# Kernel tuning notes

Measured on AMD Instinct MI355X. Metric: run time of the kernel, lower is better.

The kernel has to match this reference:

```python
import jax, jax.numpy as jnp
import numpy as np

B, N, C = 4, 4096, 1024
E = 8
K = 2
HIGH = 2            # high_noise_experts
THRESH = 0.5        # snr_threshold
CAP_FACTOR = 1.25
INTER = C * 8 // 3  # 2730


def setup_inputs() -> dict:
    key = jax.random.key(0)
    k = jax.random.split(key, 6)
    return {
        "x": jax.random.normal(k[0], (B, N, C), jnp.float32),
        "cond": jax.random.normal(k[1], (B, C), jnp.float32),
        "snr": jax.random.uniform(k[2], (B,), jnp.float32),
        "gate_w": jax.random.normal(k[3], (2 * C, E), jnp.float32) * 0.02,
        "gate_up_w": jax.random.normal(k[4], (E, C, 2 * INTER), jnp.float32) * 0.02,
        "down_w": jax.random.normal(k[5], (E, INTER, C), jnp.float32) * 0.02,
    }


def _moe_forward(x, cond, snr, gate_w, gate_up_w, down_w):
    b, n, c = x.shape
    x_flat = x.reshape(b * n, c)                       # (T, C)
    cond_flat = jnp.repeat(cond, n, axis=0)            # (T, C)
    snr_flat = jnp.repeat(snr, n)                      # (T,)

    # gating: concat(content, conditioning) -> expert logits
    logits = jnp.concatenate([x_flat, cond_flat], axis=-1) @ gate_w  # (T, E)

    # SNR mask: high-noise tokens may only use experts [0, HIGH)
    high_noise = (snr_flat < THRESH)[:, None]          # (T, 1)
    low_noise_cols = jnp.arange(E) >= HIGH             # (E,)
    logits = logits + jnp.where(high_noise & low_noise_cols, -jnp.inf, 0.0)

    # eval mode: no jitter noise
    probs = jax.nn.softmax(logits, axis=-1)            # (T, E)
    top_probs, top_idx = jax.lax.top_k(probs, K)       # (T, K)
    top_probs = top_probs / jnp.maximum(top_probs.sum(-1, keepdims=True), 1e-12)

    T = b * n
    capacity = max(1, int(CAP_FACTOR * T / E))

    def expert_fn(e, wgu, wd):
        # priority of each (token, slot) for expert e; unassigned -> -inf
        pri = jnp.where(top_idx == e, top_probs, -jnp.inf).reshape(-1)  # (T*K,)
        vals, idx = jax.lax.top_k(pri, capacity)       # capacity-limited select
        tok = idx // K                                 # token index of each slot
        w = jnp.where(jnp.isfinite(vals), vals, 0.0)   # zero weight for padding
        xe = x_flat[tok]                               # (cap, C) gather
        gu = xe @ wgu                                  # (cap, 2*INTER)
        g, u = jnp.split(gu, 2, axis=-1)
        y = (jax.nn.silu(g) * u) @ wd                  # (cap, C)
        return tok, y * w[:, None]

    toks, ys = jax.vmap(expert_fn)(jnp.arange(E), gate_up_w, down_w)
    out = jnp.zeros_like(x_flat).at[toks.reshape(-1)].add(ys.reshape(-1, c))
    return out.reshape(b, n, c)


def reference(x, cond, snr, gate_w, gate_up_w, down_w):
    out = _moe_forward(x, cond, snr, gate_w, gate_up_w, down_w)
    # eval mode: load-balance loss is 0
    return out, jnp.float32(0.0)
```

## Files before the change

### kernel.cpp

```cpp
#include <hip/hip_runtime.h>
#include <hip/hip_bf16.h>
#include <stdint.h>

#define T_TOK 16384
#define CDIM  1024
#define ENUM_ 8
#define INTER_ 2730
#define IPAD  2752
#define NGU   5460
#define NGUPAD 5504
#define CAP   2560
#define EGRP  4
#define CSTRIDE 64

typedef __attribute__((ext_vector_type(8))) short short8;
typedef __attribute__((ext_vector_type(4))) float f32x4;
typedef unsigned long long u64;
typedef unsigned int u32;

static __device__ __forceinline__ ushort f2bf(float f){
  u32 u = __float_as_uint(f);
  u32 r = u + 0x7FFFu + ((u >> 16) & 1u);
  return (ushort)(r >> 16);
}

static __device__ __forceinline__ void glds16(const void* g, void* l){
  __builtin_amdgcn_global_load_lds(
      (const __attribute__((address_space(1))) void*)g,
      (__attribute__((address_space(3))) void*)l, 16, 0, 0);
}

__global__ void k_tr_wgu(const float* __restrict__ wgu, ushort* __restrict__ wguT){
  __shared__ float tile[32][33];
  const int e = blockIdx.z;
  const int k0 = blockIdx.x*32, n0 = blockIdx.y*32;
  const float* src = wgu + (size_t)e*CDIM*NGU;
  ushort* dst = wguT + (size_t)e*NGUPAD*CDIM;
  const int tx = threadIdx.x, ty = threadIdx.y;
  #pragma unroll
  for (int r = ty; r < 32; r += 8){
    int n = n0 + tx;
    int j = (n < IPAD) ? n : n - (IPAD - INTER_);
    bool valid = (n < INTER_) || (n >= IPAD && j < NGU);
    tile[r][tx] = valid ? src[(size_t)(k0 + r)*NGU + j] : 0.f;
  }
  __syncthreads();
  #pragma unroll
  for (int r = ty; r < 32; r += 8)
    dst[(size_t)(n0 + r)*CDIM + k0 + tx] = f2bf(tile[tx][r]);
}

__global__ void k_tr_dwn(const float* __restrict__ dw, ushort* __restrict__ dwT){
  __shared__ float tile[32][33];
  const int e = blockIdx.z;
  const int k0 = blockIdx.x*32, n0 = blockIdx.y*32;
  const float* src = dw + (size_t)e*INTER_*CDIM;
  ushort* dst = dwT + (size_t)e*CDIM*IPAD;
  const int tx = threadIdx.x, ty = threadIdx.y;
  #pragma unroll
  for (int r = ty; r < 32; r += 8){
    int k = k0 + r;
    tile[r][tx] = (k < INTER_) ? src[(size_t)k*CDIM + n0 + tx] : 0.f;
  }
  __syncthreads();
  #pragma unroll
  for (int r = ty; r < 32; r += 8)
    dst[(size_t)(n0 + r)*IPAD + k0 + tx] = f2bf(tile[tx][r]);
}

__global__ void k_cond(const float* __restrict__ cond, const float* __restrict__ gate_w,
                       float* __restrict__ condlog){
  const int b = blockIdx.x;
  const int wave = threadIdx.x >> 6, lane = threadIdx.x & 63;
  float a0 = 0.f, a1 = 0.f;
  for (int c = lane; c < CDIM; c += 64){
    float cv = cond[(size_t)b*CDIM + c];
    const float* g = gate_w + (size_t)(CDIM + c)*8;
    a0 += cv * g[2*wave]; a1 += cv * g[2*wave + 1];
  }
  #pragma unroll
  for (int off = 32; off; off >>= 1){
    a0 += __shfl_down(a0, off, 64);
    a1 += __shfl_down(a1, off, 64);
  }
  if (lane == 0){
    condlog[b*8 + 2*wave]     = a0;
    condlog[b*8 + 2*wave + 1] = a1;
  }
}

__global__ __launch_bounds__(256) void k_gate(
    const float* __restrict__ x, const float* __restrict__ gate_w,
    const float* __restrict__ condlog, const float* __restrict__ snr,
    u32* __restrict__ pcnt, u64* __restrict__ entries, ushort* __restrict__ xb){
  __shared__ float gwT[8*1024];
  __shared__ u32 lcnt[8];
  __shared__ u32 lbase[8];
  __shared__ u64 keybuf[32];
  __shared__ u32 posbuf[32];
  const int tid = threadIdx.x;
  if (tid < 8) lcnt[tid] = 0;
  for (int idx = tid; idx < 8192; idx += 256){
    float v = gate_w[idx];
    gwT[(idx & 7)*1024 + (idx >> 3)] = v;
  }
  __syncthreads();
  const int wave = tid >> 6, lane = tid & 63;
  const int tbase = blockIdx.x*16 + wave*4;
  #pragma unroll 1
  for (int it = 0; it < 4; ++it){
    const int t = tbase + it;
    const int b = t >> 12;
    float acc[8] = {0,0,0,0,0,0,0,0};
    #pragma unroll
    for (int i = 0; i < 4; ++i){
      const int c = lane*4 + 256*i;
      const float4 xv = *(const float4*)(x + (size_t)t*CDIM + c);
      ushort4 xo;
      xo.x = f2bf(xv.x); xo.y = f2bf(xv.y); xo.z = f2bf(xv.z); xo.w = f2bf(xv.w);
      *(ushort4*)(xb + (size_t)t*CDIM + c) = xo;
      #pragma unroll
      for (int e = 0; e < 8; ++e){
        const float4 gv = *(const float4*)(gwT + e*1024 + c);
        acc[e] += xv.x*gv.x + xv.y*gv.y + xv.z*gv.z + xv.w*gv.w;
      }
    }
    #pragma unroll
    for (int e = 0; e < 8; ++e)
      #pragma unroll
      for (int off = 32; off; off >>= 1)
        acc[e] += __shfl_down(acc[e], off, 64);
    if (lane == 0){
      bool hn = snr[b] < 0.5f;
      float lg[8];
      #pragma unroll
      for (int e = 0; e < 8; ++e) lg[e] = acc[e] + condlog[b*8 + e];
      float mx = -1e30f;
      #pragma unroll
      for (int e = 0; e < 8; ++e) if (!(hn && e >= 2) && lg[e] > mx) mx = lg[e];
      float p[8]; float s = 0.f;
      #pragma unroll
      for (int e = 0; e < 8; ++e){ p[e] = (hn && e >= 2) ? 0.f : expf(lg[e] - mx); s += p[e]; }
      float inv = 1.f / s;
      #pragma unroll
      for (int e = 0; e < 8; ++e) p[e] *= inv;
      int i0 = 0;
      #pragma unroll
      for (int e = 1; e < 8; ++e) if (p[e] > p[i0]) i0 = e;
      int i1 = -1; float pv1 = -1.f;
      #pragma unroll
      for (int e = 0; e < 8; ++e) if (e != i0 && p[e] > pv1){ pv1 = p[e]; i1 = e; }
      float v0 = p[i0], v1 = pv1;
      float den = fmaxf(v0 + v1, 1e-12f);
      v0 /= den; v1 /= den;
      u32 flat0 = (u32)(t*2);
      const int slot = wave*4 + it;
      u32 p0 = atomicAdd(&lcnt[i0], 1u);
      u32 p1 = atomicAdd(&lcnt[i1], 1u);
      keybuf[2*slot]     = ((u64)__float_as_uint(v0) << 32) | (u64)(0xFFFFFFFFu - flat0);
      posbuf[2*slot]     = ((u32)i0 << 16) | p0;
      keybuf[2*slot + 1] = ((u64)__float_as_uint(v1) << 32) | (u64)(0xFFFFFFFFu - (flat0 + 1u));
      posbuf[2*slot + 1] = ((u32)i1 << 16) | p1;
    }
  }
  __syncthreads();
  if (tid < 8) lbase[tid] = atomicAdd(&pcnt[tid*CSTRIDE], lcnt[tid]);
  __syncthreads();
  if (tid < 32){
    u32 pe = posbuf[tid];
    int e = (int)(pe >> 16);
    u32 pos = pe & 0xFFFFu;
    entries[(size_t)e*T_TOK + lbase[e] + pos] = keybuf[tid];
  }
}

__global__ void k_select(const u32* __restrict__ pcnt, const u64* __restrict__ entries,
                         u64* __restrict__ thresh){
  const int e = blockIdx.x;
  const int n = (int)pcnt[e*CSTRIDE];
  if (n <= CAP){ if (threadIdx.x == 0) thresh[e] = 0ull; return; }
  const u64* keys = entries + (size_t)e*T_TOK;
  __shared__ u32 hist[256];
  __shared__ u64 spfx;
  __shared__ int srem;
  u64 prefix = 0, pmask = 0;
  int rem = CAP;
  for (int d = 7; d >= 0; --d){
    const int sh = d*8;
    hist[threadIdx.x] = 0;
    __syncthreads();
    for (int i = threadIdx.x; i < n; i += 256){
      u64 k = keys[i];
      if ((k & pmask) == prefix)
        atomicAdd(&hist[(u32)((k >> sh) & 0xFFull)], 1u);
    }
    __syncthreads();
    if (threadIdx.x == 0){
      int c = 0, chosen = 0, nr = rem;
      for (int v = 255; v >= 0; --v){
        int nc = c + (int)hist[v];
        if (nc >= rem){ chosen = v; nr = rem - c; break; }
        c = nc;
      }
      spfx = prefix | ((u64)(u32)chosen << sh);
      srem = nr;
    }
    __syncthreads();
    prefix = spfx; rem = srem; pmask |= (0xFFull << sh);
  }
  if (threadIdx.x == 0) thresh[e] = prefix;
}

__global__ void k_compact(const u32* __restrict__ pcnt, const u64* __restrict__ entries,
                          const u64* __restrict__ thresh, u32* __restrict__ mcnt,
                          int* __restrict__ tokbuf, float* __restrict__ wgtbuf){
  const int e = blockIdx.y;
  const int n = (int)pcnt[e*CSTRIDE];
  const u64 th = thresh[e];
  const u64* keys = entries + (size_t)e*T_TOK;
  for (int i = blockIdx.x*256 + threadIdx.x; i < n; i += gridDim.x*256){
    u64 k = keys[i];
    if (k >= th){
      u32 pos = atomicAdd(&mcnt[e], 1u);
      u32 flat = 0xFFFFFFFFu - (u32)(k & 0xFFFFFFFFull);
      tokbuf[(size_t)e*CAP + pos] = (int)(flat >> 1);
      wgtbuf[(size_t)e*CAP + pos] = __uint_as_float((u32)(k >> 32));
    }
  }
}

__global__ __launch_bounds__(256) void k_gemm1(
    const ushort* __restrict__ xb, const ushort* __restrict__ wguT_g,
    const int* __restrict__ tok_g, const u32* __restrict__ mcnt_g,
    ushort* __restrict__ h_g){
  const int z = blockIdx.z;
  const int m_e = (int)mcnt_g[z];
  const int m0 = blockIdx.x * 128;
  if (m0 >= m_e) return;
  const ushort* wguT = wguT_g + (size_t)z*NGUPAD*CDIM;
  const int* tok = tok_g + (size_t)z*CAP;
  ushort* h = h_g + (size_t)z*CAP*IPAD;
  const int j0 = blockIdx.y * 64;

  __shared__ ushort As[128*32];
  __shared__ ushort Bg[64*32];
  __shared__ ushort Bu[64*32];
  const int tid = threadIdx.x;
  const int lane = tid & 63, wave = tid >> 6;
  const int wm = wave >> 1, wn = wave & 1;
  const int lm = lane & 15, quad = lane >> 4;

  const int af0 = tid*8, af1 = tid*8 + 2048;
  const ushort* ag0 = xb + (size_t)tok[m0 + (af0 >> 5)]*CDIM + (af0 & 31);
  const ushort* ag1 = xb + (size_t)tok[m0 + (af1 >> 5)]*CDIM + (af1 & 31);
  const int br = tid >> 2, bc = (tid & 3)*8;
  const ushort* bgp = wguT + (size_t)(j0 + br)*CDIM + bc;
  const ushort* bup = wguT + (size_t)(IPAD + j0 + br)*CDIM + bc;

  f32x4 accg[4][2], accu[4][2];
  #pragma unroll
  for (int i = 0; i < 4; ++i)
    #pragma unroll
    for (int j = 0; j < 2; ++j){
      accg[i][j] = (f32x4){0.f,0.f,0.f,0.f};
      accu[i][j] = (f32x4){0.f,0.f,0.f,0.f};
    }

  for (int k0 = 0; k0 < CDIM; k0 += 32){
    glds16(ag0 + k0, As + af0);
    glds16(ag1 + k0, As + af1);
    glds16(bgp + k0, Bg + tid*8);
    glds16(bup + k0, Bu + tid*8);
    __syncthreads();
    short8 a[4], vg[2], vu[2];
    #pragma unroll
    for (int mt = 0; mt < 4; ++mt)
      a[mt] = *(const short8*)(As + (wm*64 + mt*16 + lm)*32 + quad*8);
    #pragma unroll
    for (int nt = 0; nt < 2; ++nt){
      vg[nt] = *(const short8*)(Bg + (wn*32 + nt*16 + lm)*32 + quad*8);
      vu[nt] = *(const short8*)(Bu + (wn*32 + nt*16 + lm)*32 + quad*8);
    }
    __syncthreads();
    #pragma unroll
    for (int mt = 0; mt < 4; ++mt)
      #pragma unroll
      for (int nt = 0; nt < 2; ++nt){
        accg[mt][nt] = __builtin_amdgcn_mfma_f32_16x16x32_bf16(a[mt], vg[nt], accg[mt][nt], 0, 0, 0);
        accu[mt][nt] = __builtin_amdgcn_mfma_f32_16x16x32_bf16(a[mt], vu[nt], accu[mt][nt], 0, 0, 0);
      }
  }
  #pragma unroll
  for (int mt = 0; mt < 4; ++mt)
    #pragma unroll
    for (int nt = 0; nt < 2; ++nt)
      #pragma unroll
      for (int r = 0; r < 4; ++r){
        int row = m0 + wm*64 + mt*16 + quad*4 + r;
        int col = j0 + wn*32 + nt*16 + lm;
        float g = accg[mt][nt][r];
        float uu = accu[mt][nt][r];
        float sg = g / (1.f + __expf(-g));
        h[(size_t)row*IPAD + col] = f2bf(sg * uu);
      }
}

__global__ __launch_bounds__(256) void k_gemm2(
    const ushort* __restrict__ h_g, const ushort* __restrict__ dwT_g,
    const int* __restrict__ tok_g, const float* __restrict__ wgt_g,
    const u32* __restrict__ mcnt_g, float* __restrict__ out){
  const int z = blockIdx.z;
  const int m_e = (int)mcnt_g[z];
  const int m0 = blockIdx.x * 128;
  if (m0 >= m_e) return;
  const ushort* h = h_g + (size_t)z*CAP*IPAD;
  const ushort* dwT = dwT_g + (size_t)z*CDIM*IPAD;
  const int* tok = tok_g + (size_t)z*CAP;
  const float* wgt = wgt_g + (size_t)z*CAP;
  const int n0 = blockIdx.y * 128;

  __shared__ ushort As[128*32];
  __shared__ ushort Bs[128*32];
  const int tid = threadIdx.x;
  const int lane = tid & 63, wave = tid >> 6;
  const int wm = wave >> 1, wn = wave & 1;
  const int lm = lane & 15, quad = lane >> 4;

  const int af0 = tid*8, af1 = tid*8 + 2048;
  const ushort* ap0 = h + (size_t)(m0 + (af0 >> 5))*IPAD + (af0 & 31);
  const ushort* ap1 = h + (size_t)(m0 + (af1 >> 5))*IPAD + (af1 & 31);
  const ushort* bp0 = dwT + (size_t)(n0 + (af0 >> 5))*IPAD + (af0 & 31);
  const ushort* bp1 = dwT + (size_t)(n0 + (af1 >> 5))*IPAD + (af1 & 31);

  f32x4 acc[4][4];
  #pragma unroll
  for (int i = 0; i < 4; ++i)
    #pragma unroll
    for (int j = 0; j < 4; ++j) acc[i][j] = (f32x4){0.f,0.f,0.f,0.f};

  for (int k0 = 0; k0 < IPAD; k0 += 32){
    glds16(ap0 + k0, As + af0);
    glds16(ap1 + k0, As + af1);
    glds16(bp0 + k0, Bs + af0);
    glds16(bp1 + k0, Bs + af1);
    __syncthreads();
    short8 a[4], b[4];
    #pragma unroll
    for (int mt = 0; mt < 4; ++mt)
      a[mt] = *(const short8*)(As + (wm*64 + mt*16 + lm)*32 + quad*8);
    #pragma unroll
    for (int nt = 0; nt < 4; ++nt)
      b[nt] = *(const short8*)(Bs + (wn*64 + nt*16 + lm)*32 + quad*8);
    __syncthreads();
    #pragma unroll
    for (int mt = 0; mt < 4; ++mt)
      #pragma unroll
      for (int nt = 0; nt < 4; ++nt)
        acc[mt][nt] = __builtin_amdgcn_mfma_f32_16x16x32_bf16(a[mt], b[nt], acc[mt][nt], 0, 0, 0);
  }
  #pragma unroll
  for (int mt = 0; mt < 4; ++mt)
    #pragma unroll
    for (int r = 0; r < 4; ++r){
      int row = m0 + wm*64 + mt*16 + quad*4 + r;
      float w = wgt[row];
      float* orow = out + (size_t)tok[row]*CDIM;
      #pragma unroll
      for (int nt = 0; nt < 4; ++nt){
        int col = n0 + wn*64 + nt*16 + lm;
        atomicAdd(orow + col, w * acc[mt][nt][r]);
      }
    }
}

extern "C" void kernel_launch(void* const* d_in, const int* in_sizes, int n_in,
                              void* d_out, int out_size, void* d_ws, size_t ws_size,
                              hipStream_t stream){
  const float* x      = (const float*)d_in[0];
  const float* cond   = (const float*)d_in[1];
  const float* snr    = (const float*)d_in[2];
  const float* gate_w = (const float*)d_in[3];
  const float* wgu    = (const float*)d_in[4];
  const float* wdn    = (const float*)d_in[5];
  float* out = (float*)d_out;
  (void)in_sizes; (void)n_in; (void)ws_size;

  char* ws = (char*)d_ws;
  size_t off = 0;
  auto take = [&](size_t bytes) -> char* {
    char* p = ws + off;
    off += (bytes + 255) & ~(size_t)255;
    return p;
  };
  u32* pcnt     = (u32*)take(8*CSTRIDE*4);
  u32* mcnt     = (u32*)take(256);
  float* condlog = (float*)take(256);
  u64* thresh   = (u64*)take(256);
  u64* entries  = (u64*)take((size_t)ENUM_*T_TOK*8);
  int* tokbuf   = (int*)take((size_t)ENUM_*CAP*4);
  float* wgtbuf = (float*)take((size_t)ENUM_*CAP*4);
  ushort* xb    = (ushort*)take((size_t)T_TOK*CDIM*2);
  ushort* wguT  = (ushort*)take((size_t)ENUM_*NGUPAD*CDIM*2);
  ushort* dwT   = (ushort*)take((size_t)ENUM_*CDIM*IPAD*2);
  ushort* hbuf  = (ushort*)take((size_t)EGRP*CAP*IPAD*2);

  hipMemsetAsync(pcnt, 0, 8*CSTRIDE*4, stream);
  hipMemsetAsync(mcnt, 0, 256, stream);
  hipMemsetAsync(tokbuf, 0, (size_t)ENUM_*CAP*4, stream);
  hipMemsetAsync(wgtbuf, 0, (size_t)ENUM_*CAP*4, stream);
  hipMemsetAsync(out, 0, (size_t)out_size*sizeof(float), stream);

  k_cond<<<4, 256, 0, stream>>>(cond, gate_w, condlog);
  k_gate<<<T_TOK/16, 256, 0, stream>>>(x, gate_w, condlog, snr, pcnt, entries, xb);
  k_tr_wgu<<<dim3(CDIM/32, NGUPAD/32, ENUM_), dim3(32,8), 0, stream>>>(wgu, wguT);
  k_tr_dwn<<<dim3(IPAD/32, CDIM/32, ENUM_), dim3(32,8), 0, stream>>>(wdn, dwT);
  k_select<<<ENUM_, 256, 0, stream>>>(pcnt, entries, thresh);
  k_compact<<<dim3(64, ENUM_), 256, 0, stream>>>(pcnt, entries, thresh, mcnt, tokbuf, wgtbuf);

  for (int g = 0; g < ENUM_/EGRP; ++g){
    k_gemm1<<<dim3(CAP/128, IPAD/64, EGRP), 256, 0, stream>>>(
        xb, wguT + (size_t)g*EGRP*NGUPAD*CDIM,
        tokbuf + (size_t)g*EGRP*CAP, mcnt + g*EGRP, hbuf);
    k_gemm2<<<dim3(CAP/128, CDIM/128, EGRP), 256, 0, stream>>>(
        hbuf, dwT + (size_t)g*EGRP*CDIM*IPAD,
        tokbuf + (size_t)g*EGRP*CAP, wgtbuf + (size_t)g*EGRP*CAP,
        mcnt + g*EGRP, out);
  }
}
```

Baseline: 1.045 ms.

## Replace atomic scatter-add in down-proj with per-expert buffer and token gather

The down-projection GEMM now writes unweighted per-expert outputs to a dense fp32 buffer instead of atomically adding weighted rows into the output. The compact kernel records an inverse map from each token to its (expert, slot) entries, and a new gather kernel sums the weighted rows per token and writes each output row once. This removes the float atomics and the output memset, and it merges several memsets into one range. The cost is an extra 80MB fp32 intermediate written and read back, plus one more kernel launch.

```diff
diff --git a/kernel.cpp b/kernel.cpp
--- a/kernel.cpp
+++ b/kernel.cpp
@@ -141,9 +141,9 @@
       float p[8]; float s = 0.f;
       #pragma unroll
       for (int e = 0; e < 8; ++e){ p[e] = (hn && e >= 2) ? 0.f : expf(lg[e] - mx); s += p[e]; }
-      float inv = 1.f / s;
-      #pragma unroll
-      for (int e = 0; e < 8; ++e) p[e] *= inv;
+      float inv_ = 1.f / s;
+      #pragma unroll
+      for (int e = 0; e < 8; ++e) p[e] *= inv_;
       int i0 = 0;
       #pragma unroll
       for (int e = 1; e < 8; ++e) if (p[e] > p[i0]) i0 = e;
@@ -213,7 +213,8 @@
 
 __global__ void k_compact(const u32* __restrict__ pcnt, const u64* __restrict__ entries,
                           const u64* __restrict__ thresh, u32* __restrict__ mcnt,
-                          int* __restrict__ tokbuf, float* __restrict__ wgtbuf){
+                          int* __restrict__ tokbuf, float* __restrict__ wgtbuf,
+                          u32* __restrict__ invcnt, u32* __restrict__ inv){
   const int e = blockIdx.y;
   const int n = (int)pcnt[e*CSTRIDE];
   const u64 th = thresh[e];
@@ -223,8 +224,11 @@
     if (k >= th){
       u32 pos = atomicAdd(&mcnt[e], 1u);
       u32 flat = 0xFFFFFFFFu - (u32)(k & 0xFFFFFFFFull);
-      tokbuf[(size_t)e*CAP + pos] = (int)(flat >> 1);
+      int t = (int)(flat >> 1);
+      tokbuf[(size_t)e*CAP + pos] = t;
       wgtbuf[(size_t)e*CAP + pos] = __uint_as_float((u32)(k >> 32));
+      u32 ic = atomicAdd(&invcnt[t], 1u);
+      inv[2*t + ic] = ((u32)e << 12) | pos;
     }
   }
 }
@@ -307,16 +311,13 @@
 
 __global__ __launch_bounds__(256) void k_gemm2(
     const ushort* __restrict__ h_g, const ushort* __restrict__ dwT_g,
-    const int* __restrict__ tok_g, const float* __restrict__ wgt_g,
-    const u32* __restrict__ mcnt_g, float* __restrict__ out){
+    const u32* __restrict__ mcnt_g, float* __restrict__ y_g){
   const int z = blockIdx.z;
   const int m_e = (int)mcnt_g[z];
   const int m0 = blockIdx.x * 128;
   if (m0 >= m_e) return;
   const ushort* h = h_g + (size_t)z*CAP*IPAD;
   const ushort* dwT = dwT_g + (size_t)z*CDIM*IPAD;
-  const int* tok = tok_g + (size_t)z*CAP;
-  const float* wgt = wgt_g + (size_t)z*CAP;
   const int n0 = blockIdx.y * 128;
 
   __shared__ ushort As[128*32];
@@ -363,14 +364,41 @@
     #pragma unroll
     for (int r = 0; r < 4; ++r){
       int row = m0 + wm*64 + mt*16 + quad*4 + r;
-      float w = wgt[row];
-      float* orow = out + (size_t)tok[row]*CDIM;
+      float* yrow = y_g + ((size_t)z*CAP + row)*CDIM;
       #pragma unroll
       for (int nt = 0; nt < 4; ++nt){
         int col = n0 + wn*64 + nt*16 + lm;
-        atomicAdd(orow + col, w * acc[mt][nt][r]);
+        yrow[col] = acc[mt][nt][r];
       }
     }
+}
+
+__global__ __launch_bounds__(256) void k_out(
+    const float* __restrict__ ybuf, const u32* __restrict__ inv,
+    const u32* __restrict__ invcnt, const float* __restrict__ wgtbuf,
+    float* __restrict__ out){
+  const int t = blockIdx.x*4 + (threadIdx.x >> 6);
+  const int lane = threadIdx.x & 63;
+  const int n = (int)invcnt[t];
+  f32x4 acc[4];
+  #pragma unroll
+  for (int i = 0; i < 4; ++i) acc[i] = (f32x4){0.f,0.f,0.f,0.f};
+  for (int j = 0; j < n; ++j){
+    u32 v = inv[2*t + j];
+    int e = (int)(v >> 12);
+    int pos = (int)(v & 0xFFFu);
+    float w = wgtbuf[e*CAP + pos];
+    const float* yr = ybuf + ((size_t)e*CAP + pos)*CDIM;
+    #pragma unroll
+    for (int i = 0; i < 4; ++i){
+      f32x4 yv = *(const f32x4*)(yr + i*256 + lane*4);
+      acc[i] += yv * w;
+    }
+  }
+  float* orow = out + (size_t)t*CDIM;
+  #pragma unroll
+  for (int i = 0; i < 4; ++i)
+    *(f32x4*)(orow + i*256 + lane*4) = acc[i];
 }
 
 extern "C" void kernel_launch(void* const* d_in, const int* in_sizes, int n_in,
@@ -383,7 +411,7 @@
   const float* wgu    = (const float*)d_in[4];
   const float* wdn    = (const float*)d_in[5];
   float* out = (float*)d_out;
-  (void)in_sizes; (void)n_in; (void)ws_size;
+  (void)in_sizes; (void)n_in; (void)ws_size; (void)out_size;
 
   char* ws = (char*)d_ws;
   size_t off = 0;
@@ -396,6 +424,8 @@
   u32* mcnt     = (u32*)take(256);
   float* condlog = (float*)take(256);
   u64* thresh   = (u64*)take(256);
+  u32* invcnt   = (u32*)take((size_t)T_TOK*4);
+  u32* inv      = (u32*)take((size_t)T_TOK*2*4);
   u64* entries  = (u64*)take((size_t)ENUM_*T_TOK*8);
   int* tokbuf   = (int*)take((size_t)ENUM_*CAP*4);
   float* wgtbuf = (float*)take((size_t)ENUM_*CAP*4);
@@ -403,19 +433,18 @@
   ushort* wguT  = (ushort*)take((size_t)ENUM_*NGUPAD*CDIM*2);
   ushort* dwT   = (ushort*)take((size_t)ENUM_*CDIM*IPAD*2);
   ushort* hbuf  = (ushort*)take((size_t)EGRP*CAP*IPAD*2);
-
-  hipMemsetAsync(pcnt, 0, 8*CSTRIDE*4, stream);
-  hipMemsetAsync(mcnt, 0, 256, stream);
+  float* ybuf   = (float*)take((size_t)ENUM_*CAP*CDIM*4);
+
+  hipMemsetAsync(pcnt, 0, 68352, stream);
   hipMemsetAsync(tokbuf, 0, (size_t)ENUM_*CAP*4, stream);
-  hipMemsetAsync(wgtbuf, 0, (size_t)ENUM_*CAP*4, stream);
-  hipMemsetAsync(out, 0, (size_t)out_size*sizeof(float), stream);
 
   k_cond<<<4, 256, 0, stream>>>(cond, gate_w, condlog);
   k_gate<<<T_TOK/16, 256, 0, stream>>>(x, gate_w, condlog, snr, pcnt, entries, xb);
   k_tr_wgu<<<dim3(CDIM/32, NGUPAD/32, ENUM_), dim3(32,8), 0, stream>>>(wgu, wguT);
   k_tr_dwn<<<dim3(IPAD/32, CDIM/32, ENUM_), dim3(32,8), 0, stream>>>(wdn, dwT);
   k_select<<<ENUM_, 256, 0, stream>>>(pcnt, entries, thresh);
-  k_compact<<<dim3(64, ENUM_), 256, 0, stream>>>(pcnt, entries, thresh, mcnt, tokbuf, wgtbuf);
+  k_compact<<<dim3(64, ENUM_), 256, 0, stream>>>(pcnt, entries, thresh, mcnt,
+                                                 tokbuf, wgtbuf, invcnt, inv);
 
   for (int g = 0; g < ENUM_/EGRP; ++g){
     k_gemm1<<<dim3(CAP/128, IPAD/64, EGRP), 256, 0, stream>>>(
@@ -423,7 +452,7 @@
         tokbuf + (size_t)g*EGRP*CAP, mcnt + g*EGRP, hbuf);
     k_gemm2<<<dim3(CAP/128, CDIM/128, EGRP), 256, 0, stream>>>(
         hbuf, dwT + (size_t)g*EGRP*CDIM*IPAD,
-        tokbuf + (size_t)g*EGRP*CAP, wgtbuf + (size_t)g*EGRP*CAP,
-        mcnt + g*EGRP, out);
-  }
-}
+        mcnt + g*EGRP, ybuf + (size_t)g*EGRP*CAP*CDIM);
+  }
+  k_out<<<T_TOK/4, 256, 0, stream>>>(ybuf, inv, invcnt, wgtbuf, out);
+}
```

New measurement: 1.057 ms. Within noise of the previous version (+1.2%).
